# Optimization experiments

Hardware: AMD Instinct MI355X
Metric: run time of the kernel (lower is better)

The kernel has to match this reference:

```python
import jax, jax.numpy as jnp
import numpy as np

B, S, D, H, DQK, DH = 2, 2048, 1024, 16, 64, 64

def setup_inputs() -> dict:
    key = jax.random.key(0)
    ks = jax.random.split(key, 9)
    return {
        "x":  jax.random.normal(ks[0], (B, S, D), jnp.float32),
        "Wq": jax.random.normal(ks[1], (H, D, DQK), jnp.float32) * (D ** -0.5),
        "bq": jax.random.normal(ks[2], (H, DQK), jnp.float32) * 0.02,
        "Wk": jax.random.normal(ks[3], (H, D, DQK), jnp.float32) * (D ** -0.5),
        "bk": jax.random.normal(ks[4], (H, DQK), jnp.float32) * 0.02,
        "Wv": jax.random.normal(ks[5], (H, D, DH), jnp.float32) * (D ** -0.5),
        "bv": jax.random.normal(ks[6], (H, DH), jnp.float32) * 0.02,
        "Wo": jax.random.normal(ks[7], (D, D), jnp.float32) * (D ** -0.5),
        "bo": jax.random.normal(ks[8], (D,), jnp.float32) * 0.02,
    }

def reference(x, Wq, bq, Wk, bk, Wv, bv, Wo, bo):
    b, s, d = x.shape
    # per-head projections, all heads batched: [B,H,S,*]
    Q = jnp.einsum('bsd,hde->bhse', x, Wq) + bq[None, :, None, :]
    K = jnp.einsum('bsd,hde->bhse', x, Wk) + bk[None, :, None, :]
    V = jnp.einsum('bsd,hde->bhse', x, Wv) + bv[None, :, None, :]
    scores = jnp.einsum('bhse,bhte->bhst', Q, K) * (Q.shape[-1] ** -0.5)
    causal = jnp.tril(jnp.ones((s, s), bool))
    scores = jnp.where(causal, scores, -jnp.inf)  # mask add as in torch code
    attn = jax.nn.softmax(scores, axis=-1)        # dropout p=0 (eval)
    out = jnp.einsum('bhst,bhtd->bhsd', attn, V)
    # concat heads along feature dim (head order matches torch.cat)
    out = out.transpose(0, 2, 1, 3).reshape(b, s, -1)
    return out @ Wo + bo
```

## Files before the change

### kernel.cpp

```cpp
#include <hip/hip_runtime.h>
#include <stdint.h>

typedef __attribute__((ext_vector_type(8))) short bh8;
typedef __attribute__((ext_vector_type(4))) float f32x4;
typedef __attribute__((ext_vector_type(4))) unsigned short u16x4;
typedef __attribute__((ext_vector_type(8))) unsigned short u16x8;
typedef __attribute__((ext_vector_type(2))) unsigned int u32x2;

#define DEVI static __device__ __forceinline__

constexpr int B_ = 2, S_ = 2048, D_ = 1024, H_ = 16, E_ = 64;

constexpr size_t OFF_XB  = 0;
constexpr size_t OFF_WQT = OFF_XB  + (size_t)B_*S_*D_;
constexpr size_t OFF_WKT = OFF_WQT + (size_t)H_*E_*D_;
constexpr size_t OFF_WVT = OFF_WKT + (size_t)H_*E_*D_;
constexpr size_t OFF_WOT = OFF_WVT + (size_t)H_*E_*D_;
constexpr size_t OFF_Q   = OFF_WOT + (size_t)D_*D_;
constexpr size_t OFF_K   = OFF_Q   + (size_t)B_*H_*S_*E_;
constexpr size_t OFF_VT  = OFF_K   + (size_t)B_*H_*S_*E_;
constexpr size_t OFF_O   = OFF_VT  + (size_t)B_*H_*S_*E_;

DEVI unsigned short f2bf(float f) {
    union { float f; unsigned u; } v; v.f = f;
    unsigned u = v.u;
    return (unsigned short)((u + 0x7fffu + ((u >> 16) & 1u)) >> 16);
}

DEVI unsigned cvt_pk_bf16(float lo, float hi) {
    unsigned r;
    asm("v_cvt_pk_bf16_f32 %0, %1, %2" : "=v"(r) : "v"(lo), "v"(hi));
    return r;
}

DEVI void gload16(const void* g, void* l) {
    __builtin_amdgcn_global_load_lds(
        (const __attribute__((address_space(1))) unsigned int*)g,
        (__attribute__((address_space(3))) unsigned int*)l, 16, 0, 0);
}

DEVI f32x4 mfma16(bh8 a, bh8 b, f32x4 c) {
    return __builtin_amdgcn_mfma_f32_16x16x32_bf16(a, b, c, 0, 0, 0);
}

template<int N> DEVI void vm_barrier() {
    asm volatile("s_waitcnt vmcnt(%0)" :: "i"(N) : "memory");
    __builtin_amdgcn_s_barrier();
    __builtin_amdgcn_sched_barrier(0);
}
DEVI void post_barrier() {
    __builtin_amdgcn_sched_barrier(0);
    __builtin_amdgcn_s_barrier();
    __builtin_amdgcn_sched_barrier(0);
}

__global__ __launch_bounds__(256) void k_convert_x(const float* __restrict__ x,
                                                   unsigned short* __restrict__ ws) {
    const int i = blockIdx.x * 256 + threadIdx.x;
    const float4 v = ((const float4*)x)[i];
    u16x4 o = { f2bf(v.x), f2bf(v.y), f2bf(v.z), f2bf(v.w) };
    *(u16x4*)(ws + OFF_XB + (size_t)i * 4) = o;
}

__global__ __launch_bounds__(256) void k_transpose_w(const float* __restrict__ Wq,
                                                     const float* __restrict__ Wk,
                                                     const float* __restrict__ Wv,
                                                     const float* __restrict__ Wo,
                                                     unsigned short* __restrict__ ws) {
    const int xi = blockIdx.x;
    const int z  = blockIdx.y;
    const int t  = threadIdx.x;
    __shared__ __align__(16) unsigned short tile[64][72];

    const float* src; unsigned short* dst;
    int inCols, inBase, outBase;
    if (z < 3) {
        src = (z == 0) ? Wq : (z == 1) ? Wk : Wv;
        dst = ws + ((z == 0) ? OFF_WQT : (z == 1) ? OFF_WKT : OFF_WVT);
        inCols = 64;
        inBase = xi * 64 * 64;
        const int h = xi >> 4, dt = xi & 15;
        outBase = h * 65536 + dt * 64;
    } else {
        src = Wo; dst = ws + OFF_WOT;
        inCols = 1024;
        const int et = xi >> 4, dt = xi & 15;
        inBase  = (dt * 64) * 1024 + et * 64;
        outBase = (et * 64) * 1024 + dt * 64;
    }
#pragma unroll
    for (int v = 0; v < 4; ++v) {
        const int flat = v * 256 + t;
        const int i = flat >> 4, j4 = (flat & 15) * 4;
        const float4 val = *(const float4*)(src + inBase + i * inCols + j4);
        tile[i][j4 + 0] = f2bf(val.x);
        tile[i][j4 + 1] = f2bf(val.y);
        tile[i][j4 + 2] = f2bf(val.z);
        tile[i][j4 + 3] = f2bf(val.w);
    }
    __syncthreads();
    const int j = t >> 2, iseg = (t & 3) * 16;
    u16x8 p0, p1;
#pragma unroll
    for (int u = 0; u < 8; ++u) p0[u] = tile[iseg + u][j];
#pragma unroll
    for (int u = 0; u < 8; ++u) p1[u] = tile[iseg + 8 + u][j];
    *(u16x8*)(dst + outBase + (size_t)j * 1024 + iseg)     = p0;
    *(u16x8*)(dst + outBase + (size_t)j * 1024 + iseg + 8) = p1;
}

DEVI void gemm_tile_128x128(const unsigned short* __restrict__ A,
                            const unsigned short* __restrict__ Bw,
                            unsigned short* lds,
                            f32x4 acc[2][8]) {
    const int lane = threadIdx.x & 63;
    const int w    = threadIdx.x >> 6;
    const int lr = lane & 15, lg = lane >> 4;
    const unsigned short* a0 = A  + (size_t)((w * 2 + 0) * 16 + lr) * D_ + lg * 8;
    const unsigned short* a1 = A  + (size_t)((w * 2 + 1) * 16 + lr) * D_ + lg * 8;
    const unsigned short* b0 = Bw + (size_t)((w * 2 + 0) * 16 + lr) * D_ + lg * 8;
    const unsigned short* b1 = Bw + (size_t)((w * 2 + 1) * 16 + lr) * D_ + lg * 8;
    const int oA0 = (w * 2 + 0) * 512, oA1 = (w * 2 + 1) * 512;
    const int oB0 = 4096 + oA0,        oB1 = 4096 + oA1;

    auto stage = [&](int ks, int bufi) {
        unsigned short* base = lds + bufi * 8192;
        gload16(a0 + ks * 32, base + oA0);
        gload16(a1 + ks * 32, base + oA1);
        gload16(b0 + ks * 32, base + oB0);
        gload16(b1 + ks * 32, base + oB1);
    };

    stage(0, 0); stage(1, 1); stage(2, 2);
    for (int ks = 0; ks < 32; ++ks) {
        if (ks < 30)       vm_barrier<8>();
        else if (ks == 30) vm_barrier<4>();
        else               vm_barrier<0>();
        const unsigned short* base = lds + (ks % 3) * 8192;
        bh8 af0 = *(const bh8*)(base + (w * 2 + 0) * 512 + lane * 8);
        bh8 af1 = *(const bh8*)(base + (w * 2 + 1) * 512 + lane * 8);
#pragma unroll
        for (int nt = 0; nt < 8; ++nt) {
            bh8 bf = *(const bh8*)(base + 4096 + nt * 512 + lane * 8);
            acc[0][nt] = mfma16(af0, bf, acc[0][nt]);
            acc[1][nt] = mfma16(af1, bf, acc[1][nt]);
        }
        post_barrier();
        if (ks + 3 < 32) stage(ks + 3, ks % 3);
    }
}

__global__ __launch_bounds__(256, 3) void k_qkv(unsigned short* __restrict__ ws,
                                                const float* __restrict__ bq,
                                                const float* __restrict__ bk,
                                                const float* __restrict__ bv) {
    const int flat  = blockIdx.x;
    const int idx   = flat >> 3;
    const int stile = (flat & 7) * 4 + (idx & 3);
    const int ntile = idx >> 2;
    const int row0  = stile * 128;
    const unsigned short* A  = ws + OFF_XB  + (size_t)row0 * D_;
    const unsigned short* Bw = ws + OFF_WQT + (size_t)ntile * 128 * D_;

    __shared__ __align__(16) unsigned short lds[3 * 8192];
    f32x4 acc[2][8];
#pragma unroll
    for (int i = 0; i < 2; ++i)
#pragma unroll
        for (int j = 0; j < 8; ++j) acc[i][j] = (f32x4){0.f, 0.f, 0.f, 0.f};

    gemm_tile_128x128(A, Bw, lds, acc);

    const int lane = threadIdx.x & 63, w = threadIdx.x >> 6;
    const int lr = lane & 15, lg = lane >> 4;
    const int srow0 = row0 + w * 32;
    const int b     = srow0 >> 11;
    const int sl0   = srow0 & (S_ - 1);
#pragma unroll
    for (int mt = 0; mt < 2; ++mt) {
#pragma unroll
        for (int nt = 0; nt < 8; ++nt) {
            const int gcol = ntile * 128 + nt * 16;
            const int mat  = gcol >> 10;
            const int h    = (gcol >> 6) & 15;
            const int e    = (gcol & 63) + lr;
            const int bh   = b * H_ + h;
            const float bia = ((mat == 0) ? bq : (mat == 1) ? bk : bv)[h * 64 + e];
            if (mat == 0) {
                u16x4 pk;
#pragma unroll
                for (int r = 0; r < 4; ++r)
                    pk[r] = f2bf((acc[mt][nt][r] + bia) * 0.1803368801f);
                const int sl = sl0 + mt * 16 + lg * 4;
                *(u16x4*)(ws + OFF_Q + ((size_t)(bh * E_ + e)) * S_ + sl) = pk;
            } else if (mat == 2) {
                u16x4 pk;
#pragma unroll
                for (int r = 0; r < 4; ++r) pk[r] = f2bf(acc[mt][nt][r] + bia);
                const int sl = sl0 + mt * 16 + lg * 4;
                *(u16x4*)(ws + OFF_VT + ((size_t)(bh * E_ + e)) * S_ + sl) = pk;
            } else {
#pragma unroll
                for (int r = 0; r < 4; ++r) {
                    const int sl = sl0 + mt * 16 + lg * 4 + r;
                    ws[OFF_K + ((size_t)bh * S_ + sl) * E_ + e] = f2bf(acc[mt][nt][r] + bia);
                }
            }
        }
    }
}

__global__ __launch_bounds__(256, 4) void k_attn(unsigned short* __restrict__ ws) {
    const int flat = blockIdx.x;
    const int j    = flat & 31;
    const int qt   = 31 - (flat >> 5);
    const int bh   = (j & 7) * 4 + (j >> 3);
    const int lane = threadIdx.x & 63, w = threadIdx.x >> 6;
    const int lr = lane & 15, lg = lane >> 4;
    const unsigned short* Qp = ws + OFF_Q  + (size_t)bh * E_ * S_;
    const unsigned short* Kp = ws + OFF_K  + (size_t)bh * S_ * E_;
    const unsigned short* Vp = ws + OFF_VT + (size_t)bh * E_ * S_;
    __shared__ __align__(16) unsigned short ldsK[2][8 * 512];
    __shared__ __align__(16) unsigned short ldsV[2][8 * 512];
    __shared__ __align__(16) unsigned short ldsP[4 * 1024];

    const int qbase = qt * 64 + w * 16;
    bh8 qf[2];
#pragma unroll
    for (int kg = 0; kg < 2; ++kg) {
        bh8 t;
#pragma unroll
        for (int i = 0; i < 8; ++i)
            t[i] = (short)Qp[(size_t)(kg * 32 + lg * 8 + i) * S_ + qbase + lr];
        qf[kg] = t;
    }

    f32x4 o[4];
    float m = -3.0e38f, l = 0.f;
#pragma unroll
    for (int i = 0; i < 4; ++i) o[i] = (f32x4){0.f, 0.f, 0.f, 0.f};

    auto stage = [&](int kt, int bufi) {
        const int sk0 = kt * 64;
#pragma unroll
        for (int u = 0; u < 2; ++u) {
            const int blk = w * 2 + u;
            const int ct = blk >> 1, kg = blk & 1;
            gload16(Kp + (size_t)(sk0 + ct * 16 + lr) * E_ + kg * 32 + lg * 8,
                    &ldsK[bufi][blk * 512]);
            gload16(Vp + (size_t)(ct * 16 + lr) * S_ + sk0 + kg * 32 + lg * 8,
                    &ldsV[bufi][blk * 512]);
        }
    };

    unsigned short* Pw = ldsP + w * 1024;

    stage(0, 0);
    if (qt >= 1) stage(1, 1);

    for (int kt = 0; kt <= qt; ++kt) {
        if (kt < qt) vm_barrier<4>();
        else         vm_barrier<0>();
        const int cur = kt & 1;
        const unsigned short* Kc = ldsK[cur];
        const unsigned short* Vc = ldsV[cur];

        f32x4 sc[4];
#pragma unroll
        for (int ct = 0; ct < 4; ++ct) sc[ct] = (f32x4){0.f, 0.f, 0.f, 0.f};
#pragma unroll
        for (int ct = 0; ct < 4; ++ct)
#pragma unroll
            for (int kg = 0; kg < 2; ++kg) {
                bh8 kf = *(const bh8*)(Kc + (ct * 2 + kg) * 512 + lane * 8);
                sc[ct] = mfma16(kf, qf[kg], sc[ct]);
            }
        if (kt == qt) {
#pragma unroll
            for (int ct = 0; ct < 4; ++ct) {
                const int skl = ct * 16 + lg * 4;
#pragma unroll
                for (int r = 0; r < 4; ++r)
                    if (skl + r > w * 16 + lr) sc[ct][r] = -3.0e38f;
            }
        }
        float mx = fmaxf(fmaxf(sc[0][0], sc[0][1]), fmaxf(sc[0][2], sc[0][3]));
#pragma unroll
        for (int ct = 1; ct < 4; ++ct)
            mx = fmaxf(mx, fmaxf(fmaxf(sc[ct][0], sc[ct][1]),
                                 fmaxf(sc[ct][2], sc[ct][3])));
        mx = fmaxf(mx, __shfl_xor(mx, 16, 64));
        mx = fmaxf(mx, __shfl_xor(mx, 32, 64));
        const bool need = mx > m + 8.0f;
        if (__any(need)) {
            const float mn = need ? mx : m;
            const float sf = __builtin_amdgcn_exp2f(m - mn);
            m = mn;
            l *= sf;
#pragma unroll
            for (int r = 0; r < 4; ++r) {
                const float sfq = __shfl(sf, (lane & 48) + lg * 4 + r, 64);
#pragma unroll
                for (int et = 0; et < 4; ++et) o[et][r] *= sfq;
            }
        }
        float rs = 0.f;
#pragma unroll
        for (int ct = 0; ct < 4; ++ct)
#pragma unroll
            for (int r = 0; r < 4; ++r) {
                float p = __builtin_amdgcn_exp2f(sc[ct][r] - m);
                sc[ct][r] = p;
                rs += p;
            }
        rs += __shfl_xor(rs, 16, 64);
        rs += __shfl_xor(rs, 32, 64);
        l += rs;
#pragma unroll
        for (int ct = 0; ct < 4; ++ct) {
            u32x2 pk = { cvt_pk_bf16(sc[ct][0], sc[ct][1]),
                         cvt_pk_bf16(sc[ct][2], sc[ct][3]) };
            const int addr = (ct >> 1) * 512 +
                             ((((ct & 1) * 2) + (lg >> 1)) * 16 + lr) * 8 + (lg & 1) * 4;
            *(u32x2*)(Pw + addr) = pk;
        }
#pragma unroll
        for (int skg = 0; skg < 2; ++skg) {
            bh8 pf = *(const bh8*)(Pw + skg * 512 + lane * 8);
#pragma unroll
            for (int et = 0; et < 4; ++et) {
                bh8 vf = *(const bh8*)(Vc + (et * 2 + skg) * 512 + lane * 8);
                o[et] = mfma16(pf, vf, o[et]);
            }
        }
        post_barrier();
        if (kt + 2 <= qt) stage(kt + 2, cur);
    }
    const int b = bh >> 4, hh = bh & 15;
#pragma unroll
    for (int r = 0; r < 4; ++r) {
        const float lq = __shfl(l, (lane & 48) + lg * 4 + r, 64);
        const float inv = 1.0f / lq;
        const int s = qbase + lg * 4 + r;
#pragma unroll
        for (int et = 0; et < 4; ++et)
            ws[OFF_O + ((size_t)(b * S_ + s)) * D_ + hh * E_ + et * 16 + lr] =
                f2bf(o[et][r] * inv);
    }
}

__global__ __launch_bounds__(256, 3) void k_oproj(const unsigned short* __restrict__ ws,
                                                  const float* __restrict__ bo,
                                                  float* __restrict__ out) {
    const int flat  = blockIdx.x;
    const int idx   = flat >> 3;
    const int stile = (flat & 7) * 4 + (idx & 3);
    const int ntile = idx >> 2;
    const unsigned short* A  = ws + OFF_O   + (size_t)stile * 128 * D_;
    const unsigned short* Bw = ws + OFF_WOT + (size_t)ntile * 128 * D_;
    __shared__ __align__(16) unsigned short lds[3 * 8192];
    f32x4 acc[2][8];
#pragma unroll
    for (int i = 0; i < 2; ++i)
#pragma unroll
        for (int j = 0; j < 8; ++j) acc[i][j] = (f32x4){0.f, 0.f, 0.f, 0.f};

    gemm_tile_128x128(A, Bw, lds, acc);

    const int lane = threadIdx.x & 63, w = threadIdx.x >> 6;
    const int lr = lane & 15, lg = lane >> 4;
    const int r0 = stile * 128 + w * 32;
#pragma unroll
    for (int mt = 0; mt < 2; ++mt)
#pragma unroll
        for (int nt = 0; nt < 8; ++nt) {
            const int e = ntile * 128 + nt * 16 + lr;
            const float bia = bo[e];
#pragma unroll
            for (int r = 0; r < 4; ++r)
                out[(size_t)(r0 + mt * 16 + lg * 4 + r) * D_ + e] = acc[mt][nt][r] + bia;
        }
}

extern "C" void kernel_launch(void* const* d_in, const int* in_sizes, int n_in,
                              void* d_out, int out_size, void* d_ws, size_t ws_size,
                              hipStream_t stream) {
    const float* x  = (const float*)d_in[0];
    const float* Wq = (const float*)d_in[1];
    const float* bq = (const float*)d_in[2];
    const float* Wk = (const float*)d_in[3];
    const float* bk = (const float*)d_in[4];
    const float* Wv = (const float*)d_in[5];
    const float* bv = (const float*)d_in[6];
    const float* Wo = (const float*)d_in[7];
    const float* bo = (const float*)d_in[8];
    float* out = (float*)d_out;
    unsigned short* ws = (unsigned short*)d_ws;

    k_convert_x<<<dim3((B_ * S_ * D_) / 4 / 256), 256, 0, stream>>>(x, ws);
    k_transpose_w<<<dim3(256, 4), 256, 0, stream>>>(Wq, Wk, Wv, Wo, ws);
    k_qkv<<<dim3(768), 256, 0, stream>>>(ws, bq, bk, bv);
    k_attn<<<dim3(1024), 256, 0, stream>>>(ws);
    k_oproj<<<dim3(256), 256, 0, stream>>>(ws, bo, out);
}
```

Measured before the change: 129.2 us.

## Shrink QKV and output-projection GEMM tiles to 128x64 with double buffering

Changes the shared GEMM tile from 128x128 with triple-buffered LDS to 128x64 with double buffering. This doubles the grid of the QKV and output-projection kernels and raises launch bounds to 6 blocks per CU. The goal is better CU occupancy and load balance, since the output projection previously launched only 256 blocks. In exchange each block reuses less of the A tile, so A traffic per FLOP goes up, and the shallower pipeline may expose more load latency.

```diff
diff --git a/kernel.cpp b/kernel.cpp
--- a/kernel.cpp
+++ b/kernel.cpp
@@ -109,83 +109,80 @@
     *(u16x8*)(dst + outBase + (size_t)j * 1024 + iseg + 8) = p1;
 }
 
-DEVI void gemm_tile_128x128(const unsigned short* __restrict__ A,
-                            const unsigned short* __restrict__ Bw,
-                            unsigned short* lds,
-                            f32x4 acc[2][8]) {
+DEVI void gemm_tile_128x64(const unsigned short* __restrict__ A,
+                           const unsigned short* __restrict__ Bw,
+                           unsigned short* lds,
+                           f32x4 acc[2][4]) {
     const int lane = threadIdx.x & 63;
     const int w    = threadIdx.x >> 6;
     const int lr = lane & 15, lg = lane >> 4;
     const unsigned short* a0 = A  + (size_t)((w * 2 + 0) * 16 + lr) * D_ + lg * 8;
     const unsigned short* a1 = A  + (size_t)((w * 2 + 1) * 16 + lr) * D_ + lg * 8;
-    const unsigned short* b0 = Bw + (size_t)((w * 2 + 0) * 16 + lr) * D_ + lg * 8;
-    const unsigned short* b1 = Bw + (size_t)((w * 2 + 1) * 16 + lr) * D_ + lg * 8;
-    const int oA0 = (w * 2 + 0) * 512, oA1 = (w * 2 + 1) * 512;
-    const int oB0 = 4096 + oA0,        oB1 = 4096 + oA1;
+    const unsigned short* b0 = Bw + (size_t)(w * 16 + lr) * D_ + lg * 8;
+    const int oA0 = (w * 2 + 0) * 512, oA1 = (w * 2 + 1) * 512, oB = 8 * 512 + w * 512;
 
     auto stage = [&](int ks, int bufi) {
-        unsigned short* base = lds + bufi * 8192;
+        unsigned short* base = lds + bufi * 6144;
         gload16(a0 + ks * 32, base + oA0);
         gload16(a1 + ks * 32, base + oA1);
-        gload16(b0 + ks * 32, base + oB0);
-        gload16(b1 + ks * 32, base + oB1);
+        gload16(b0 + ks * 32, base + oB);
     };
 
-    stage(0, 0); stage(1, 1); stage(2, 2);
+    stage(0, 0); stage(1, 1);
     for (int ks = 0; ks < 32; ++ks) {
-        if (ks < 30)       vm_barrier<8>();
-        else if (ks == 30) vm_barrier<4>();
-        else               vm_barrier<0>();
-        const unsigned short* base = lds + (ks % 3) * 8192;
+        if (ks < 31) vm_barrier<3>();
+        else         vm_barrier<0>();
+        const unsigned short* base = lds + (ks & 1) * 6144;
         bh8 af0 = *(const bh8*)(base + (w * 2 + 0) * 512 + lane * 8);
         bh8 af1 = *(const bh8*)(base + (w * 2 + 1) * 512 + lane * 8);
 #pragma unroll
-        for (int nt = 0; nt < 8; ++nt) {
-            bh8 bf = *(const bh8*)(base + 4096 + nt * 512 + lane * 8);
+        for (int nt = 0; nt < 4; ++nt) {
+            bh8 bf = *(const bh8*)(base + 8 * 512 + nt * 512 + lane * 8);
             acc[0][nt] = mfma16(af0, bf, acc[0][nt]);
             acc[1][nt] = mfma16(af1, bf, acc[1][nt]);
         }
         post_barrier();
-        if (ks + 3 < 32) stage(ks + 3, ks % 3);
-    }
-}
-
-__global__ __launch_bounds__(256, 3) void k_qkv(unsigned short* __restrict__ ws,
+        if (ks + 2 < 32) stage(ks + 2, ks & 1);
+    }
+}
+
+__global__ __launch_bounds__(256, 6) void k_qkv(unsigned short* __restrict__ ws,
                                                 const float* __restrict__ bq,
                                                 const float* __restrict__ bk,
                                                 const float* __restrict__ bv) {
     const int flat  = blockIdx.x;
+    const int xcd   = flat & 7;
     const int idx   = flat >> 3;
-    const int stile = (flat & 7) * 4 + (idx & 3);
+    const int stile = xcd * 4 + (idx & 3);
     const int ntile = idx >> 2;
     const int row0  = stile * 128;
+    const int mat   = ntile >> 4;
+    const int h     = ntile & 15;
     const unsigned short* A  = ws + OFF_XB  + (size_t)row0 * D_;
-    const unsigned short* Bw = ws + OFF_WQT + (size_t)ntile * 128 * D_;
-
-    __shared__ __align__(16) unsigned short lds[3 * 8192];
-    f32x4 acc[2][8];
+    const unsigned short* Bw = ws + OFF_WQT + (size_t)ntile * 64 * D_;
+    const float* bias = ((mat == 0) ? bq : (mat == 1) ? bk : bv) + h * 64;
+
+    __shared__ __align__(16) unsigned short lds[2 * 6144];
+    f32x4 acc[2][4];
 #pragma unroll
     for (int i = 0; i < 2; ++i)
 #pragma unroll
-        for (int j = 0; j < 8; ++j) acc[i][j] = (f32x4){0.f, 0.f, 0.f, 0.f};
-
-    gemm_tile_128x128(A, Bw, lds, acc);
+        for (int j = 0; j < 4; ++j) acc[i][j] = (f32x4){0.f, 0.f, 0.f, 0.f};
+
+    gemm_tile_128x64(A, Bw, lds, acc);
 
     const int lane = threadIdx.x & 63, w = threadIdx.x >> 6;
     const int lr = lane & 15, lg = lane >> 4;
     const int srow0 = row0 + w * 32;
     const int b     = srow0 >> 11;
     const int sl0   = srow0 & (S_ - 1);
+    const int bh    = b * H_ + h;
 #pragma unroll
     for (int mt = 0; mt < 2; ++mt) {
 #pragma unroll
-        for (int nt = 0; nt < 8; ++nt) {
-            const int gcol = ntile * 128 + nt * 16;
-            const int mat  = gcol >> 10;
-            const int h    = (gcol >> 6) & 15;
-            const int e    = (gcol & 63) + lr;
-            const int bh   = b * H_ + h;
-            const float bia = ((mat == 0) ? bq : (mat == 1) ? bk : bv)[h * 64 + e];
+        for (int nt = 0; nt < 4; ++nt) {
+            const int e = nt * 16 + lr;
+            const float bia = bias[e];
             if (mat == 0) {
                 u16x4 pk;
 #pragma unroll
@@ -349,23 +346,24 @@
     }
 }
 
-__global__ __launch_bounds__(256, 3) void k_oproj(const unsigned short* __restrict__ ws,
+__global__ __launch_bounds__(256, 6) void k_oproj(const unsigned short* __restrict__ ws,
                                                   const float* __restrict__ bo,
                                                   float* __restrict__ out) {
     const int flat  = blockIdx.x;
+    const int xcd   = flat & 7;
     const int idx   = flat >> 3;
-    const int stile = (flat & 7) * 4 + (idx & 3);
+    const int stile = xcd * 4 + (idx & 3);
     const int ntile = idx >> 2;
     const unsigned short* A  = ws + OFF_O   + (size_t)stile * 128 * D_;
-    const unsigned short* Bw = ws + OFF_WOT + (size_t)ntile * 128 * D_;
-    __shared__ __align__(16) unsigned short lds[3 * 8192];
-    f32x4 acc[2][8];
+    const unsigned short* Bw = ws + OFF_WOT + (size_t)ntile * 64 * D_;
+    __shared__ __align__(16) unsigned short lds[2 * 6144];
+    f32x4 acc[2][4];
 #pragma unroll
     for (int i = 0; i < 2; ++i)
 #pragma unroll
-        for (int j = 0; j < 8; ++j) acc[i][j] = (f32x4){0.f, 0.f, 0.f, 0.f};
-
-    gemm_tile_128x128(A, Bw, lds, acc);
+        for (int j = 0; j < 4; ++j) acc[i][j] = (f32x4){0.f, 0.f, 0.f, 0.f};
+
+    gemm_tile_128x64(A, Bw, lds, acc);
 
     const int lane = threadIdx.x & 63, w = threadIdx.x >> 6;
     const int lr = lane & 15, lg = lane >> 4;
@@ -373,8 +371,8 @@
 #pragma unroll
     for (int mt = 0; mt < 2; ++mt)
 #pragma unroll
-        for (int nt = 0; nt < 8; ++nt) {
-            const int e = ntile * 128 + nt * 16 + lr;
+        for (int nt = 0; nt < 4; ++nt) {
+            const int e = ntile * 64 + nt * 16 + lr;
             const float bia = bo[e];
 #pragma unroll
             for (int r = 0; r < 4; ++r)
@@ -399,7 +397,7 @@
 
     k_convert_x<<<dim3((B_ * S_ * D_) / 4 / 256), 256, 0, stream>>>(x, ws);
     k_transpose_w<<<dim3(256, 4), 256, 0, stream>>>(Wq, Wk, Wv, Wo, ws);
-    k_qkv<<<dim3(768), 256, 0, stream>>>(ws, bq, bk, bv);
+    k_qkv<<<dim3(1536), 256, 0, stream>>>(ws, bq, bk, bv);
     k_attn<<<dim3(1024), 256, 0, stream>>>(ws);
-    k_oproj<<<dim3(256), 256, 0, stream>>>(ws, bo, out);
-}
+    k_oproj<<<dim3(512), 256, 0, stream>>>(ws, bo, out);
+}
```

Result: slower. 154.4 us (+19.6%).
